# Kernel tuning notes

Hardware: AMD Instinct MI355X
Metric: run time of the kernel (lower is better)

## Reference

```python
import jax, jax.numpy as jnp
import numpy as np

N = 50000          # nodes
E = 800000         # edges (before self-loops)
IN_CH = 128
H1, C1 = 8, 32     # layer-1 heads / channels-per-head (concat -> 256)
H2, C2 = 1, 64     # layer-2 (out_channels=64, heads=1)
NEG_SLOPE = 0.2    # PyG GATConv default LeakyReLU slope for attention


def setup_inputs() -> dict:
    key = jax.random.key(0)
    ks = jax.random.split(key, 10)
    x = jax.random.normal(ks[0], (N, IN_CH), dtype=jnp.float32)
    edge_index = jax.random.randint(ks[1], (2, E), 0, N, dtype=jnp.int64)
    s = 0.05
    W1 = jax.random.normal(ks[2], (IN_CH, H1 * C1), dtype=jnp.float32) * s
    a_src1 = jax.random.normal(ks[3], (H1, C1), dtype=jnp.float32) * s
    a_dst1 = jax.random.normal(ks[4], (H1, C1), dtype=jnp.float32) * s
    b1 = jnp.zeros((H1 * C1,), dtype=jnp.float32)
    W2 = jax.random.normal(ks[5], (H1 * C1, H2 * C2), dtype=jnp.float32) * s
    a_src2 = jax.random.normal(ks[6], (H2, C2), dtype=jnp.float32) * s
    a_dst2 = jax.random.normal(ks[7], (H2, C2), dtype=jnp.float32) * s
    b2 = jnp.zeros((H2 * C2,), dtype=jnp.float32)
    return {"x": x, "edge_index": edge_index,
            "W1": W1, "a_src1": a_src1, "a_dst1": a_dst1, "b1": b1,
            "W2": W2, "a_src2": a_src2, "a_dst2": a_dst2, "b2": b2}


def gat_conv(x, src, dst, W, a_src, a_dst, b, heads, ch):
    """PyG GATConv (eval mode): gather -> LeakyReLU attn -> scatter-softmax -> scatter-add."""
    n = x.shape[0]
    h = (x @ W).reshape(n, heads, ch)                     # [N, H, C]
    alpha_s = jnp.einsum('nhc,hc->nh', h, a_src)          # [N, H]
    alpha_d = jnp.einsum('nhc,hc->nh', h, a_dst)
    e = jax.nn.leaky_relu(alpha_s[src] + alpha_d[dst], NEG_SLOPE)  # [E, H]
    # numerically-stable softmax over edges grouped by destination node
    emax = jax.ops.segment_max(e, dst, num_segments=n)
    e = jnp.exp(e - emax[dst])
    denom = jax.ops.segment_sum(e, dst, num_segments=n)
    alpha = e / denom[dst]                                # [E, H]
    out = jax.ops.segment_sum(h[src] * alpha[:, :, None], dst, num_segments=n)  # [N, H, C]
    return out.reshape(n, heads * ch) + b


def reference(x, edge_index, W1, a_src1, a_dst1, b1, W2, a_src2, a_dst2, b2):
    # PyG GATConv adds self-loops by default
    loops = jnp.arange(N, dtype=edge_index.dtype)
    src = jnp.concatenate([edge_index[0], loops])
    dst = jnp.concatenate([edge_index[1], loops])
    h = jax.nn.relu(gat_conv(x, src, dst, W1, a_src1, a_dst1, b1, H1, C1))
    out = jax.nn.relu(gat_conv(h, src, dst, W2, a_src2, a_dst2, b2, H2, C2))
    return out
```

## Files before the change

### kernel.cpp

```cpp
#include <hip/hip_runtime.h>
#include <math.h>

#define NEG_SLOPE 0.2f
__device__ __forceinline__ float leaky(float x) { return fmaxf(x, NEG_SLOPE * x); }

typedef _Float16 f16;
typedef _Float16 f16x2 __attribute__((ext_vector_type(2)));
typedef _Float16 f16x4 __attribute__((ext_vector_type(4)));
typedef _Float16 f16x8 __attribute__((ext_vector_type(8)));
typedef float f32x4 __attribute__((ext_vector_type(4)));

__device__ __forceinline__ int kmap(int lh, int e) {
  return (e < 4) ? lh * 4 + e : 16 + lh * 4 + (e - 4);
}

__global__ void k_count(const int* __restrict__ dst, int* __restrict__ deg, int E) {
  int e = blockIdx.x * blockDim.x + threadIdx.x;
  if (e < E) atomicAdd(&deg[dst[e]], 1);
}

#define W1_TOT (17 * 4 * 64 * 8)
#define W2_TOT (5 * 8 * 64 * 8)
__global__ __launch_bounds__(256) void k_partial_packw(const int* __restrict__ deg,
    int* __restrict__ part, int n, int nb,
    const float* __restrict__ W1, const float* __restrict__ as1f,
    const float* __restrict__ ad1f, const float* __restrict__ W2,
    const float* __restrict__ as2f, const float* __restrict__ ad2f,
    f16* __restrict__ Wp1, f16* __restrict__ Wp2) {
  if ((int)blockIdx.x < nb) {
    __shared__ int s[256];
    int i = blockIdx.x * 256 + threadIdx.x;
    s[threadIdx.x] = (i < n) ? deg[i] : 0;
    __syncthreads();
    for (int off = 128; off > 0; off >>= 1) {
      if (threadIdx.x < off) s[threadIdx.x] += s[threadIdx.x + off];
      __syncthreads();
    }
    if (threadIdx.x == 0) part[blockIdx.x] = s[0];
  }
  int tid = blockIdx.x * 256 + threadIdx.x;
  if (tid < W1_TOT) {
    int e = tid & 7, l = (tid >> 3) & 63, ks = (tid >> 9) & 3, nt = tid >> 11;
    int lh = l >> 4, li = l & 15;
    int k = ks * 32 + kmap(lh, e);
    float v;
    if (nt < 16) {
      v = W1[k * 256 + nt * 16 + li];
    } else {
      int h = li & 7;
      const float* a = (li < 8) ? (as1f + h * 32) : (ad1f + h * 32);
      v = 0.f;
      for (int j = 0; j < 32; ++j) v += W1[k * 256 + h * 32 + j] * a[j];
    }
    Wp1[tid] = (f16)v;
  } else if (tid < W1_TOT + W2_TOT) {
    int t2 = tid - W1_TOT;
    int e = t2 & 7, l = (t2 >> 3) & 63, ks = (t2 >> 9) & 7, nt = t2 >> 12;
    int lh = l >> 4, li = l & 15;
    int k = ks * 32 + kmap(lh, e);
    float v = 0.f;
    if (nt < 4) {
      v = W2[k * 64 + nt * 16 + li];
    } else if (li == 0) {
      for (int j = 0; j < 64; ++j) v += W2[k * 64 + j] * as2f[j];
    } else if (li == 1) {
      for (int j = 0; j < 64; ++j) v += W2[k * 64 + j] * ad2f[j];
    }
    Wp2[t2] = (f16)v;
  }
}

__global__ __launch_bounds__(256) void k_offs(int* __restrict__ deg,
                                              const int* __restrict__ part,
                                              int* __restrict__ offs, int n, int nb) {
  __shared__ int ps[256];
  __shared__ int s[256];
  int t = threadIdx.x;
  ps[t] = (t < nb) ? part[t] : 0;
  __syncthreads();
  for (int off = 1; off < 256; off <<= 1) {
    int u = (t >= off) ? ps[t - off] : 0;
    __syncthreads();
    ps[t] += u;
    __syncthreads();
  }
  int base = (blockIdx.x > 0) ? ps[blockIdx.x - 1] : 0;

  int i = blockIdx.x * 256 + t;
  int v = (i < n) ? deg[i] : 0;
  s[t] = v;
  __syncthreads();
  for (int off = 1; off < 256; off <<= 1) {
    int u = (t >= off) ? s[t - off] : 0;
    __syncthreads();
    s[t] += u;
    __syncthreads();
  }
  int excl = base + s[t] - v;
  if (i < n) {
    offs[i] = excl;
    deg[i] = 0;
  }
  if (i == n - 1) offs[n] = excl + v;
}

__global__ void k_fill(const int* __restrict__ src, const int* __restrict__ dst,
                       const int* __restrict__ offs, int* __restrict__ cursor,
                       int* __restrict__ col, int E) {
  int e = blockIdx.x * blockDim.x + threadIdx.x;
  if (e >= E) return;
  int d = dst[e];
  int pos = atomicAdd(&cursor[d], 1);
  col[offs[d] + pos] = src[e];
}

__global__ __launch_bounds__(256) void k_gemm1(const float* __restrict__ x,
    const f16* __restrict__ Wp1, f16* __restrict__ h16,
    float* __restrict__ as, float* __restrict__ ad, int n, int nSlots) {
  int slot = blockIdx.x * 4 + (threadIdx.x >> 6);
  if (slot >= nSlots) return;
  int half = slot & 1;
  int wid = slot >> 1;
  int lane = threadIdx.x & 63, lh = lane >> 4, li = lane & 15;
  size_t arow = (size_t)min(wid * 16 + li, n - 1);
  f16x8 a[4];
#pragma unroll
  for (int ks = 0; ks < 4; ++ks) {
    float4 lo = *(const float4*)&x[arow * 128 + ks * 32 + lh * 4];
    float4 hi = *(const float4*)&x[arow * 128 + ks * 32 + 16 + lh * 4];
    a[ks][0] = (f16)lo.x; a[ks][1] = (f16)lo.y; a[ks][2] = (f16)lo.z; a[ks][3] = (f16)lo.w;
    a[ks][4] = (f16)hi.x; a[ks][5] = (f16)hi.y; a[ks][6] = (f16)hi.z; a[ks][7] = (f16)hi.w;
  }
  int rbase = wid * 16 + lh * 4;
  int ntBeg = half ? 8 : 0;
  int ntEnd = half ? 17 : 8;
  for (int nt = ntBeg; nt < ntEnd; ++nt) {
    f32x4 acc = {0.f, 0.f, 0.f, 0.f};
#pragma unroll
    for (int ks = 0; ks < 4; ++ks) {
      f16x8 b = *(const f16x8*)&Wp1[((nt * 4 + ks) * 64 + lane) * 8];
      acc = __builtin_amdgcn_mfma_f32_16x16x32_f16(a[ks], b, acc, 0, 0, 0);
    }
    if (nt < 16) {
#pragma unroll
      for (int r = 0; r < 4; ++r) {
        int rr = rbase + r;
        if (rr < n) h16[(size_t)rr * 256 + nt * 16 + li] = (f16)acc[r];
      }
    } else {
#pragma unroll
      for (int r = 0; r < 4; ++r) {
        int rr = rbase + r;
        if (rr < n) {
          if (li < 8) as[(size_t)rr * 8 + li] = acc[r];
          else        ad[(size_t)rr * 8 + (li - 8)] = acc[r];
        }
      }
    }
  }
}

__global__ __launch_bounds__(256) void k_gemm2(const f16* __restrict__ R16,
    const f16* __restrict__ Wp2, f16* __restrict__ h2,
    float* __restrict__ as, float* __restrict__ ad, int n, int nWaves) {
  int wid = blockIdx.x * 4 + (threadIdx.x >> 6);
  if (wid >= nWaves) return;
  int lane = threadIdx.x & 63, lh = lane >> 4, li = lane & 15;
  size_t arow = (size_t)min(wid * 16 + li, n - 1);
  f16x8 a[8];
#pragma unroll
  for (int ks = 0; ks < 8; ++ks) {
    f16x4 lo = *(const f16x4*)&R16[arow * 256 + ks * 32 + lh * 4];
    f16x4 hi = *(const f16x4*)&R16[arow * 256 + ks * 32 + 16 + lh * 4];
    a[ks][0] = lo[0]; a[ks][1] = lo[1]; a[ks][2] = lo[2]; a[ks][3] = lo[3];
    a[ks][4] = hi[0]; a[ks][5] = hi[1]; a[ks][6] = hi[2]; a[ks][7] = hi[3];
  }
  int rbase = wid * 16 + lh * 4;
#pragma unroll
  for (int nt = 0; nt < 5; ++nt) {
    f32x4 acc = {0.f, 0.f, 0.f, 0.f};
#pragma unroll
    for (int ks = 0; ks < 8; ++ks) {
      f16x8 b = *(const f16x8*)&Wp2[((nt * 8 + ks) * 64 + lane) * 8];
      acc = __builtin_amdgcn_mfma_f32_16x16x32_f16(a[ks], b, acc, 0, 0, 0);
    }
    if (nt < 4) {
#pragma unroll
      for (int r = 0; r < 4; ++r) {
        int rr = rbase + r;
        if (rr < n) h2[(size_t)rr * 64 + nt * 16 + li] = (f16)acc[r];
      }
    } else {
#pragma unroll
      for (int r = 0; r < 4; ++r) {
        int rr = rbase + r;
        if (rr < n) {
          if (li == 0) as[rr] = acc[r];
          else if (li == 1) ad[rr] = acc[r];
        }
      }
    }
  }
}

#define DEPTH1 16
__global__ __launch_bounds__(256) void k_agg1(const f16* __restrict__ h16,
    const float* __restrict__ as, const float* __restrict__ ad,
    const int* __restrict__ offs, const int* __restrict__ col,
    const float* __restrict__ b, f16* __restrict__ out, int n) {
  int node = blockIdx.x * 4 + (threadIdx.x >> 6);
  if (node >= n) return;
  node = __builtin_amdgcn_readfirstlane(node);
  int lane = threadIdx.x & 63;
  int head = lane >> 3;
  int c0 = lane * 4;
  int beg = offs[node], end = offs[node + 1];
  float adn = ad[node * 8 + head];

  float denom, ax, ay, az, aw;
  {
    float w = __expf(leaky(as[node * 8 + head] + adn));
    f16x4 g = *(const f16x4*)&h16[(size_t)node * 256 + c0];
    denom = w;
    ax = w * (float)g[0]; ay = w * (float)g[1];
    az = w * (float)g[2]; aw = w * (float)g[3];
  }
  for (int p = beg; p < end; p += DEPTH1) {
    int cnt = end - p;
    int s[DEPTH1];
#pragma unroll
    for (int j = 0; j < DEPTH1; ++j) s[j] = (j < cnt) ? col[p + j] : node;
    float e[DEPTH1];
#pragma unroll
    for (int j = 0; j < DEPTH1; ++j) e[j] = as[s[j] * 8 + head];
    f16x4 g[DEPTH1];
#pragma unroll
    for (int j = 0; j < DEPTH1; ++j) g[j] = *(const f16x4*)&h16[(size_t)s[j] * 256 + c0];
    float w[DEPTH1];
#pragma unroll
    for (int j = 0; j < DEPTH1; ++j) w[j] = (j < cnt) ? __expf(leaky(e[j] + adn)) : 0.f;
#pragma unroll
    for (int j = 0; j < DEPTH1; ++j) {
      denom += w[j];
      ax += w[j] * (float)g[j][0]; ay += w[j] * (float)g[j][1];
      az += w[j] * (float)g[j][2]; aw += w[j] * (float)g[j][3];
    }
  }
  float inv = 1.f / denom;
  float4 bv = *(const float4*)&b[c0];
  f16x4 o;
  o[0] = (f16)fmaxf(fmaf(ax, inv, bv.x), 0.f);
  o[1] = (f16)fmaxf(fmaf(ay, inv, bv.y), 0.f);
  o[2] = (f16)fmaxf(fmaf(az, inv, bv.z), 0.f);
  o[3] = (f16)fmaxf(fmaf(aw, inv, bv.w), 0.f);
  __builtin_nontemporal_store(o, (f16x4*)&out[(size_t)node * 256 + c0]);
}

__global__ __launch_bounds__(256) void k_agg2(const f16* __restrict__ h2,
    const float* __restrict__ as, const float* __restrict__ ad,
    const int* __restrict__ offs, const int* __restrict__ col,
    const float* __restrict__ b, float* __restrict__ out, int n) {
  int node = blockIdx.x * 4 + (threadIdx.x >> 6);
  if (node >= n) return;
  node = __builtin_amdgcn_readfirstlane(node);
  int lane = threadIdx.x & 63;
  int es = lane >> 4;
  int c = lane & 15;
  int beg = offs[node], end = offs[node + 1];
  int deg = end - beg;
  float adn = ad[node];

  float a0 = 0.f, a1 = 0.f, a2 = 0.f, a3 = 0.f, wsum = 0.f;
  if (es == 0) {
    float w = __expf(leaky(as[node] + adn));
    f16x4 g = *(const f16x4*)&h2[(size_t)node * 64 + c * 4];
    wsum = w;
    a0 = w * (float)g[0]; a1 = w * (float)g[1];
    a2 = w * (float)g[2]; a3 = w * (float)g[3];
  }
  for (int base = 0; base < deg; base += 16) {
    int s[4]; float e[4]; f16x4 g[4]; float w[4];
#pragma unroll
    for (int q = 0; q < 4; ++q) {
      int idx = base + q * 4 + es;
      s[q] = (idx < deg) ? col[beg + idx] : node;
    }
#pragma unroll
    for (int q = 0; q < 4; ++q) e[q] = as[s[q]];
#pragma unroll
    for (int q = 0; q < 4; ++q) g[q] = *(const f16x4*)&h2[(size_t)s[q] * 64 + c * 4];
#pragma unroll
    for (int q = 0; q < 4; ++q) {
      int idx = base + q * 4 + es;
      w[q] = (idx < deg) ? __expf(leaky(e[q] + adn)) : 0.f;
    }
#pragma unroll
    for (int q = 0; q < 4; ++q) {
      wsum += w[q];
      a0 += w[q] * (float)g[q][0]; a1 += w[q] * (float)g[q][1];
      a2 += w[q] * (float)g[q][2]; a3 += w[q] * (float)g[q][3];
    }
  }
  a0 += __shfl_xor(a0, 16, 64); a1 += __shfl_xor(a1, 16, 64);
  a2 += __shfl_xor(a2, 16, 64); a3 += __shfl_xor(a3, 16, 64);
  wsum += __shfl_xor(wsum, 16, 64);
  a0 += __shfl_xor(a0, 32, 64); a1 += __shfl_xor(a1, 32, 64);
  a2 += __shfl_xor(a2, 32, 64); a3 += __shfl_xor(a3, 32, 64);
  wsum += __shfl_xor(wsum, 32, 64);
  if (es == 0) {
    float inv = 1.f / wsum;
    float4 bv = *(const float4*)&b[c * 4];
    f32x4 o;
    o[0] = fmaxf(fmaf(a0, inv, bv.x), 0.f);
    o[1] = fmaxf(fmaf(a1, inv, bv.y), 0.f);
    o[2] = fmaxf(fmaf(a2, inv, bv.z), 0.f);
    o[3] = fmaxf(fmaf(a3, inv, bv.w), 0.f);
    __builtin_nontemporal_store(o, (f32x4*)&out[(size_t)node * 64 + c * 4]);
  }
}

extern "C" void kernel_launch(void* const* d_in, const int* in_sizes, int n_in,
                              void* d_out, int out_size, void* d_ws, size_t ws_size,
                              hipStream_t stream) {
  const float* x      = (const float*)d_in[0];
  const int*   ei     = (const int*)d_in[1];
  const float* W1     = (const float*)d_in[2];
  const float* a_src1 = (const float*)d_in[3];
  const float* a_dst1 = (const float*)d_in[4];
  const float* b1     = (const float*)d_in[5];
  const float* W2     = (const float*)d_in[6];
  const float* a_src2 = (const float*)d_in[7];
  const float* a_dst2 = (const float*)d_in[8];
  const float* b2     = (const float*)d_in[9];

  int N = in_sizes[0] / 128;
  int E = in_sizes[1] / 2;
  const int* srcI = ei;
  const int* dstI = ei + E;
  int nb = (N + 255) / 256;
  int packBlocks = (W1_TOT + W2_TOT + 255) / 256;
  int ppBlocks = nb > packBlocks ? nb : packBlocks;
  int nWaves = (N + 15) / 16;
  int nSlots1 = nWaves * 2;
  int nodeBlocks = (N + 3) / 4;

  char* ws = (char*)d_ws;
  size_t o = 0;
  auto alloc = [&](size_t bytes) -> void* {
    void* p = ws + o;
    o += (bytes + 255) & ~(size_t)255;
    return p;
  };
  f16*   h1f    = (f16*)alloc((size_t)N * 256 * 2);
  f16*   r16    = (f16*)alloc((size_t)N * 256 * 2);
  f16*   h2f    = (f16*)alloc((size_t)N * 64 * 2);
  f16*   Wp1    = (f16*)alloc((size_t)W1_TOT * 2);
  f16*   Wp2    = (f16*)alloc((size_t)W2_TOT * 2);
  float* as1    = (float*)alloc((size_t)N * 8 * 4);
  float* ad1    = (float*)alloc((size_t)N * 8 * 4);
  float* as2    = (float*)alloc((size_t)N * 4);
  float* ad2    = (float*)alloc((size_t)N * 4);
  int*   offs   = (int*)alloc((size_t)(N + 1) * 4);
  int*   cursor = (int*)alloc((size_t)N * 4);
  int*   col    = (int*)alloc((size_t)E * 4);
  int*   part   = (int*)alloc((size_t)nb * 4);

  hipMemsetAsync(cursor, 0, (size_t)N * 4, stream);
  k_count<<<(E + 255) / 256, 256, 0, stream>>>(dstI, cursor, E);
  k_partial_packw<<<ppBlocks, 256, 0, stream>>>(cursor, part, N, nb,
      W1, a_src1, a_dst1, W2, a_src2, a_dst2, Wp1, Wp2);
  k_offs<<<nb, 256, 0, stream>>>(cursor, part, offs, N, nb);
  k_fill<<<(E + 255) / 256, 256, 0, stream>>>(srcI, dstI, offs, cursor, col, E);

  k_gemm1<<<(nSlots1 + 3) / 4, 256, 0, stream>>>(x, Wp1, h1f, as1, ad1, N, nSlots1);
  k_agg1<<<nodeBlocks, 256, 0, stream>>>(h1f, as1, ad1, offs, col, b1, r16, N);

  k_gemm2<<<(nWaves + 3) / 4, 256, 0, stream>>>(r16, Wp2, h2f, as2, ad2, N, nWaves);
  k_agg2<<<nodeBlocks, 256, 0, stream>>>(h2f, as2, ad2, offs, col, b2, (float*)d_out, N);
}
```

Before: 220.1 us.

## Fuse CSR fill with layer-1 GEMM launch and tighten agg1 neighbor loop

The CSR fill and the layer-1 GEMM are independent, so they now run as one launch that partitions blocks between them. This removes a kernel boundary and lets the atomic-bound fill overlap with the MFMA GEMM. Separately, the layer-1 aggregation loop changes from a predicated depth-16 batch to an unpredicated 8-wide batch with a scalar tail. Short neighbor lists (about 17 on average) then stop paying for padded self-gathers, at the cost of less memory-level parallelism per iteration.

After: 216.0 us. No clear change (-1.9%).

```diff
diff --git a/kernel.cpp b/kernel.cpp
--- a/kernel.cpp
+++ b/kernel.cpp
@@ -104,20 +104,22 @@
   if (i == n - 1) offs[n] = excl + v;
 }
 
-__global__ void k_fill(const int* __restrict__ src, const int* __restrict__ dst,
-                       const int* __restrict__ offs, int* __restrict__ cursor,
-                       int* __restrict__ col, int E) {
-  int e = blockIdx.x * blockDim.x + threadIdx.x;
-  if (e >= E) return;
-  int d = dst[e];
-  int pos = atomicAdd(&cursor[d], 1);
-  col[offs[d] + pos] = src[e];
-}
-
-__global__ __launch_bounds__(256) void k_gemm1(const float* __restrict__ x,
-    const f16* __restrict__ Wp1, f16* __restrict__ h16,
-    float* __restrict__ as, float* __restrict__ ad, int n, int nSlots) {
-  int slot = blockIdx.x * 4 + (threadIdx.x >> 6);
+__global__ __launch_bounds__(256) void k_fill_gemm1(
+    const int* __restrict__ src, const int* __restrict__ dst,
+    const int* __restrict__ offs, int* __restrict__ cursor,
+    int* __restrict__ col, int E, int fillBlocks,
+    const float* __restrict__ x, const f16* __restrict__ Wp1,
+    f16* __restrict__ h16, float* __restrict__ as, float* __restrict__ ad,
+    int n, int nSlots) {
+  if ((int)blockIdx.x < fillBlocks) {
+    int e = blockIdx.x * 256 + threadIdx.x;
+    if (e >= E) return;
+    int d = dst[e];
+    int pos = atomicAdd(&cursor[d], 1);
+    col[offs[d] + pos] = src[e];
+    return;
+  }
+  int slot = (blockIdx.x - fillBlocks) * 4 + (threadIdx.x >> 6);
   if (slot >= nSlots) return;
   int half = slot & 1;
   int wid = slot >> 1;
@@ -203,7 +205,6 @@
   }
 }
 
-#define DEPTH1 16
 __global__ __launch_bounds__(256) void k_agg1(const f16* __restrict__ h16,
     const float* __restrict__ as, const float* __restrict__ ad,
     const int* __restrict__ offs, const int* __restrict__ col,
@@ -225,26 +226,34 @@
     ax = w * (float)g[0]; ay = w * (float)g[1];
     az = w * (float)g[2]; aw = w * (float)g[3];
   }
-  for (int p = beg; p < end; p += DEPTH1) {
-    int cnt = end - p;
-    int s[DEPTH1];
-#pragma unroll
-    for (int j = 0; j < DEPTH1; ++j) s[j] = (j < cnt) ? col[p + j] : node;
-    float e[DEPTH1];
-#pragma unroll
-    for (int j = 0; j < DEPTH1; ++j) e[j] = as[s[j] * 8 + head];
-    f16x4 g[DEPTH1];
-#pragma unroll
-    for (int j = 0; j < DEPTH1; ++j) g[j] = *(const f16x4*)&h16[(size_t)s[j] * 256 + c0];
-    float w[DEPTH1];
-#pragma unroll
-    for (int j = 0; j < DEPTH1; ++j) w[j] = (j < cnt) ? __expf(leaky(e[j] + adn)) : 0.f;
-#pragma unroll
-    for (int j = 0; j < DEPTH1; ++j) {
+  int p = beg;
+  for (; p + 8 <= end; p += 8) {
+    int s[8];
+#pragma unroll
+    for (int j = 0; j < 8; ++j) s[j] = col[p + j];
+    float e[8];
+#pragma unroll
+    for (int j = 0; j < 8; ++j) e[j] = as[s[j] * 8 + head];
+    f16x4 g[8];
+#pragma unroll
+    for (int j = 0; j < 8; ++j) g[j] = *(const f16x4*)&h16[(size_t)s[j] * 256 + c0];
+    float w[8];
+#pragma unroll
+    for (int j = 0; j < 8; ++j) w[j] = __expf(leaky(e[j] + adn));
+#pragma unroll
+    for (int j = 0; j < 8; ++j) {
       denom += w[j];
       ax += w[j] * (float)g[j][0]; ay += w[j] * (float)g[j][1];
       az += w[j] * (float)g[j][2]; aw += w[j] * (float)g[j][3];
     }
+  }
+  for (; p < end; ++p) {
+    int s = col[p];
+    float w = __expf(leaky(as[s * 8 + head] + adn));
+    f16x4 g = *(const f16x4*)&h16[(size_t)s * 256 + c0];
+    denom += w;
+    ax += w * (float)g[0]; ay += w * (float)g[1];
+    az += w * (float)g[2]; aw += w * (float)g[3];
   }
   float inv = 1.f / denom;
   float4 bv = *(const float4*)&b[c0];
@@ -342,6 +351,8 @@
   int ppBlocks = nb > packBlocks ? nb : packBlocks;
   int nWaves = (N + 15) / 16;
   int nSlots1 = nWaves * 2;
+  int fillBlocks = (E + 255) / 256;
+  int gemm1Blocks = (nSlots1 + 3) / 4;
   int nodeBlocks = (N + 3) / 4;
 
   char* ws = (char*)d_ws;
@@ -370,9 +381,11 @@
   k_partial_packw<<<ppBlocks, 256, 0, stream>>>(cursor, part, N, nb,
       W1, a_src1, a_dst1, W2, a_src2, a_dst2, Wp1, Wp2);
   k_offs<<<nb, 256, 0, stream>>>(cursor, part, offs, N, nb);
-  k_fill<<<(E + 255) / 256, 256, 0, stream>>>(srcI, dstI, offs, cursor, col, E);
-
-  k_gemm1<<<(nSlots1 + 3) / 4, 256, 0, stream>>>(x, Wp1, h1f, as1, ad1, N, nSlots1);
+
+  k_fill_gemm1<<<fillBlocks + gemm1Blocks, 256, 0, stream>>>(
+      srcI, dstI, offs, cursor, col, E, fillBlocks,
+      x, Wp1, h1f, as1, ad1, N, nSlots1);
+
   k_agg1<<<nodeBlocks, 256, 0, stream>>>(h1f, as1, ad1, offs, col, b1, r16, N);
 
   k_gemm2<<<(nWaves + 3) / 4, 256, 0, stream>>>(r16, Wp2, h2f, as2, ad2, N, nWaves);
```
